# Kernel tuning notes

Hardware: AMD Instinct MI355X
Metric: run time of the kernel (lower is better)

Reference implementation:

```python
import jax, jax.numpy as jnp
import numpy as np

DIM = 512
HEADS = 16
HEAD_DIM = DIM // HEADS
SCALE = HEAD_DIM ** -0.5           # qk_scale defaults to head_dim**-0.5
W_GAIN = 1.0 / np.sqrt(DIM)        # FullyConnectedLayer weight_gain (lr_multiplier=1)


def _fc(x, w, b):
    # FullyConnectedLayer: x @ (w * weight_gain).T + b  (linear activation, bias_gain=1)
    return x @ (w * W_GAIN).T + b


def setup_inputs() -> dict:
    key = jax.random.key(0)
    ks = jax.random.split(key, 12)
    B_, N = 2048, 64
    nW = 64
    x = jax.random.normal(ks[0], (B_, N, DIM), dtype=jnp.float32)
    mask = jax.random.normal(ks[1], (nW, N, N), dtype=jnp.float32)
    mask_windows = jax.random.randint(ks[2], (B_, N, 1), 0, 2).astype(jnp.float32)
    # learned params: torch.randn init for weights, bias init 0
    qw = jax.random.normal(ks[3], (DIM, DIM), dtype=jnp.float32)
    kw = jax.random.normal(ks[4], (DIM, DIM), dtype=jnp.float32)
    vw = jax.random.normal(ks[5], (DIM, DIM), dtype=jnp.float32)
    pw = jax.random.normal(ks[6], (DIM, DIM), dtype=jnp.float32)
    qb = jnp.zeros((DIM,), jnp.float32)
    kb = jnp.zeros((DIM,), jnp.float32)
    vb = jnp.zeros((DIM,), jnp.float32)
    pb = jnp.zeros((DIM,), jnp.float32)
    return {"x": x, "mask": mask, "mask_windows": mask_windows,
            "qw": qw, "qb": qb, "kw": kw, "kb": kb,
            "vw": vw, "vb": vb, "pw": pw, "pb": pb}


def reference(x, mask, mask_windows, qw, qb, kw, kb, vw, vb, pw, pb):
    B, N, C = x.shape
    H, hd = HEADS, HEAD_DIM
    # F.normalize(p=2, dim=-1) with eps=1e-12 clamp on the norm
    norm = jnp.maximum(jnp.linalg.norm(x, axis=-1, keepdims=True), 1e-12)
    nx = x / norm
    q = _fc(nx, qw, qb).reshape(B, N, H, hd).transpose(0, 2, 1, 3)   # bhnd
    k = _fc(nx, kw, kb).reshape(B, N, H, hd).transpose(0, 2, 3, 1)   # bhdn
    v = _fc(x, vw, vb).reshape(B, N, H, hd).transpose(0, 2, 1, 3)    # bhnd
    attn = (q @ k) * SCALE                                           # [B,H,N,N]
    # shifted-window additive mask, broadcast over heads
    nW = mask.shape[0]
    attn = attn.reshape(B // nW, nW, H, N, N) + mask[None, :, None, :, :]
    attn = attn.reshape(B, H, N, N)
    # token-validity mask: 0 -> -100, 1 -> 0 (values are exactly 0/1)
    amw = mask_windows[:, :, 0][:, None, None, :]                    # [B,1,1,N]
    attn = attn + jnp.where(amw == 0, jnp.float32(-100.0), jnp.float32(0.0))
    attn = jax.nn.softmax(attn, axis=-1)
    out = (attn @ v).transpose(0, 2, 1, 3).reshape(B, N, C)
    out = _fc(out, pw, pb)
    # updated mask_windows (no-grad path in original)
    mw = jnp.clip(jnp.sum(mask_windows, axis=1, keepdims=True), 0.0, 1.0)  # [B,1,1]
    mw = jnp.tile(mw, (1, N, 1))                                           # [B,N,1]
    return out, mw
```

## Files before the change

kernel.cpp:

```cpp
#include <hip/hip_runtime.h>
#include <hip/hip_bf16.h>
#include <stdint.h>

typedef __bf16 bf16_t;
typedef bf16_t bf16x8 __attribute__((ext_vector_type(8)));
typedef float  f32x4  __attribute__((ext_vector_type(4)));

#define DEV static __device__ __forceinline__

constexpr int   BATCH  = 2048;
constexpr int   SEQ    = 64;
constexpr int   DIMC   = 512;
constexpr int   HEADS  = 16;
constexpr int   M_ROWS = BATCH * SEQ;
constexpr float W_GAIN = 0.044194173824159216f;
constexpr float QK_SCALE = 0.17677669529663687f;

DEV void async_copy16(const void* gp, void* lp) {
  __builtin_amdgcn_global_load_lds((__attribute__((address_space(1))) void*)(gp),
                                   (__attribute__((address_space(3))) void*)(lp),
                                   16, 0, 0);
}

DEV f32x4 mfma16(bf16x8 a, bf16x8 b, f32x4 c) {
  return __builtin_amdgcn_mfma_f32_16x16x32_bf16(a, b, c, 0, 0, 0);
}

__global__ __launch_bounds__(256) void k_prep(const float* __restrict__ x,
                                              bf16_t* __restrict__ nx,
                                              float* __restrict__ norms) {
  const int wid = threadIdx.x >> 6, lane = threadIdx.x & 63;
  const int row = blockIdx.x * 4 + wid;
  const float4* xr = (const float4*)(x + (size_t)row * DIMC);
  float4 v0 = xr[lane * 2 + 0];
  float4 v1 = xr[lane * 2 + 1];
  float ss = v0.x*v0.x + v0.y*v0.y + v0.z*v0.z + v0.w*v0.w
           + v1.x*v1.x + v1.y*v1.y + v1.z*v1.z + v1.w*v1.w;
#pragma unroll
  for (int o = 1; o < 64; o <<= 1) ss += __shfl_xor(ss, o);
  const float nrm = fmaxf(sqrtf(ss), 1e-12f);
  const float inv = 1.0f / nrm;
  bf16x8 o;
  o[0] = (bf16_t)(v0.x * inv); o[1] = (bf16_t)(v0.y * inv);
  o[2] = (bf16_t)(v0.z * inv); o[3] = (bf16_t)(v0.w * inv);
  o[4] = (bf16_t)(v1.x * inv); o[5] = (bf16_t)(v1.y * inv);
  o[6] = (bf16_t)(v1.z * inv); o[7] = (bf16_t)(v1.w * inv);
  *(bf16x8*)(nx + (size_t)row * DIMC + lane * 8) = o;
  if (lane == 0) norms[row] = nrm;
}

__global__ __launch_bounds__(256) void k_convw(const float* __restrict__ qw,
                                               const float* __restrict__ kw,
                                               const float* __restrict__ vw,
                                               const float* __restrict__ pw,
                                               bf16_t* __restrict__ wqkv,
                                               bf16_t* __restrict__ pwb) {
  const int i = blockIdx.x * 256 + threadIdx.x;
  constexpr int QKV_ELEMS = 1536 * 512;
  if (i < QKV_ELEMS) {
    const int n = i >> 9;
    float v = (n < 512) ? qw[i] : (n < 1024) ? kw[i - 512 * 512] : vw[i - 1024 * 512];
    wqkv[i] = (bf16_t)(v * W_GAIN);
  } else {
    const int j = i - QKV_ELEMS;
    pwb[j] = (bf16_t)(pw[j] * W_GAIN);
  }
}

template <int MODE>
__global__ __launch_bounds__(256) void k_gemm(const bf16_t* __restrict__ A,
                                              const bf16_t* __restrict__ Bw,
                                              const float* __restrict__ norms,
                                              const float* __restrict__ qb,
                                              const float* __restrict__ kb,
                                              const float* __restrict__ vb,
                                              bf16_t* __restrict__ Cb,
                                              float* __restrict__ Cf,
                                              const float* __restrict__ pb,
                                              int ntiles_n) {
  __shared__ bf16_t As[128 * 32];
  __shared__ bf16_t Bs[128 * 32];
  const int tid  = threadIdx.x;
  const int wid  = tid >> 6, lane = tid & 63;
  const int tn   = blockIdx.x % ntiles_n;
  const int tm   = blockIdx.x / ntiles_n;
  const int m0   = tm * 128, n0 = tn * 128;
  const int c    = lane & 15, g = lane >> 4;
  const int wr   = (wid >> 1) * 64, wc = (wid & 1) * 64;
  const int sr0  = wid * 16 + (lane >> 2);
  const int kc8  = (lane & 3) * 8;

  f32x4 acc[4][4] = {};

  for (int kt = 0; kt < 16; ++kt) {
    const int k0 = kt * 32;
    async_copy16(A  + (size_t)(m0 + sr0)      * 512 + k0 + kc8, &As[(wid    ) * 512]);
    async_copy16(A  + (size_t)(m0 + 64 + sr0) * 512 + k0 + kc8, &As[(4 + wid) * 512]);
    async_copy16(Bw + (size_t)(n0 + sr0)      * 512 + k0 + kc8, &Bs[(wid    ) * 512]);
    async_copy16(Bw + (size_t)(n0 + 64 + sr0) * 512 + k0 + kc8, &Bs[(4 + wid) * 512]);
    __syncthreads();

    bf16x8 af[4], bfr[4];
#pragma unroll
    for (int mi = 0; mi < 4; ++mi)
      af[mi] = *(const bf16x8*)&As[(wr + mi * 16 + c) * 32 + g * 8];
#pragma unroll
    for (int nj = 0; nj < 4; ++nj)
      bfr[nj] = *(const bf16x8*)&Bs[(wc + nj * 16 + c) * 32 + g * 8];
#pragma unroll
    for (int mi = 0; mi < 4; ++mi)
#pragma unroll
      for (int nj = 0; nj < 4; ++nj)
        acc[mi][nj] = mfma16(af[mi], bfr[nj], acc[mi][nj]);
    __syncthreads();
  }

  if (MODE == 0) {
#pragma unroll
    for (int mi = 0; mi < 4; ++mi) {
#pragma unroll
      for (int r = 0; r < 4; ++r) {
        const int gm = m0 + wr + mi * 16 + g * 4 + r;
        const float nrm = norms[gm];
#pragma unroll
        for (int nj = 0; nj < 4; ++nj) {
          const int gn = n0 + wc + nj * 16 + c;
          const float bias = (gn < 512) ? qb[gn] : (gn < 1024) ? kb[gn - 512] : vb[gn - 1024];
          float v = acc[mi][nj][r];
          if (gn >= 1024) v *= nrm;
          v += bias;
          Cb[(size_t)gm * 1536 + gn] = (bf16_t)v;
        }
      }
    }
  } else {
#pragma unroll
    for (int mi = 0; mi < 4; ++mi)
#pragma unroll
      for (int nj = 0; nj < 4; ++nj) {
        const int gn = n0 + wc + nj * 16 + c;
        const float bias = pb[gn];
#pragma unroll
        for (int r = 0; r < 4; ++r) {
          const int gm = m0 + wr + mi * 16 + g * 4 + r;
          Cf[(size_t)gm * 512 + gn] = acc[mi][nj][r] + bias;
        }
      }
  }
}

__global__ __launch_bounds__(256) void k_attn(const bf16_t* __restrict__ qkv,
                                              const float* __restrict__ wmask,
                                              const float* __restrict__ mwin,
                                              bf16_t* __restrict__ aout) {
  __shared__ bf16_t Pl[4][64 * 72];
  __shared__ bf16_t Vl[4][64 * 34];
  const int wid = threadIdx.x >> 6, lane = threadIdx.x & 63;
  const int gw  = blockIdx.x * 4 + wid;
  const int b   = gw >> 4, h = gw & 15;
  const int c   = lane & 15, g = lane >> 4;
  const size_t base = (size_t)b * 64 * 1536;

  bf16x8 qa[4], kf[4];
#pragma unroll
  for (int mi = 0; mi < 4; ++mi)
    qa[mi] = *(const bf16x8*)(qkv + base + (size_t)(mi * 16 + c) * 1536 + h * 32 + g * 8);
#pragma unroll
  for (int nj = 0; nj < 4; ++nj)
    kf[nj] = *(const bf16x8*)(qkv + base + (size_t)(nj * 16 + c) * 1536 + 512 + h * 32 + g * 8);

  {
    const int jr = lane >> 2;
    const int c8 = (lane & 3) * 8;
#pragma unroll
    for (int t = 0; t < 4; ++t) {
      const int row = jr + t * 16;
      bf16x8 v = *(const bf16x8*)(qkv + base + (size_t)row * 1536 + 1024 + h * 32 + c8);
      uint32_t* dst = (uint32_t*)&Vl[wid][row * 34 + c8];
      const uint32_t* src = (const uint32_t*)&v;
      dst[0] = src[0]; dst[1] = src[1]; dst[2] = src[2]; dst[3] = src[3];
    }
  }

  f32x4 s[4][4];
  const f32x4 zero = {0.f, 0.f, 0.f, 0.f};
#pragma unroll
  for (int mi = 0; mi < 4; ++mi)
#pragma unroll
    for (int nj = 0; nj < 4; ++nj)
      s[mi][nj] = mfma16(qa[mi], kf[nj], zero);

  float kadd[4];
#pragma unroll
  for (int nj = 0; nj < 4; ++nj) {
    const float mv = mwin[b * 64 + nj * 16 + c];
    kadd[nj] = (mv == 0.0f) ? -100.0f : 0.0f;
  }
  const int w = b & 63;
  const float* wm = wmask + (size_t)w * 4096;
#pragma unroll
  for (int mi = 0; mi < 4; ++mi)
#pragma unroll
    for (int nj = 0; nj < 4; ++nj)
#pragma unroll
      for (int r = 0; r < 4; ++r) {
        const int i = mi * 16 + g * 4 + r;
        s[mi][nj][r] = s[mi][nj][r] * QK_SCALE + wm[i * 64 + nj * 16 + c] + kadd[nj];
      }

#pragma unroll
  for (int mi = 0; mi < 4; ++mi)
#pragma unroll
    for (int r = 0; r < 4; ++r) {
      float mx = fmaxf(fmaxf(s[mi][0][r], s[mi][1][r]), fmaxf(s[mi][2][r], s[mi][3][r]));
#pragma unroll
      for (int o = 1; o < 16; o <<= 1) mx = fmaxf(mx, __shfl_xor(mx, o));
      float sum = 0.f;
#pragma unroll
      for (int nj = 0; nj < 4; ++nj) {
        const float p = __expf(s[mi][nj][r] - mx);
        s[mi][nj][r] = p;
        sum += p;
      }
#pragma unroll
      for (int o = 1; o < 16; o <<= 1) sum += __shfl_xor(sum, o);
      const float inv = 1.0f / sum;
#pragma unroll
      for (int nj = 0; nj < 4; ++nj) s[mi][nj][r] *= inv;
    }

#pragma unroll
  for (int mi = 0; mi < 4; ++mi)
#pragma unroll
    for (int nj = 0; nj < 4; ++nj)
#pragma unroll
      for (int r = 0; r < 4; ++r) {
        const int i = mi * 16 + g * 4 + r, j = nj * 16 + c;
        Pl[wid][i * 72 + j] = (bf16_t)s[mi][nj][r];
      }
  f32x4 o[4][2] = {};
#pragma unroll
  for (int ks = 0; ks < 2; ++ks) {
    bf16x8 pa[4];
#pragma unroll
    for (int mi = 0; mi < 4; ++mi)
      pa[mi] = *(const bf16x8*)&Pl[wid][(mi * 16 + c) * 72 + ks * 32 + g * 8];
#pragma unroll
    for (int nd = 0; nd < 2; ++nd) {
      bf16x8 vf;
#pragma unroll
      for (int t = 0; t < 8; ++t)
        vf[t] = Vl[wid][(ks * 32 + g * 8 + t) * 34 + nd * 16 + c];
#pragma unroll
      for (int mi = 0; mi < 4; ++mi)
        o[mi][nd] = mfma16(pa[mi], vf, o[mi][nd]);
    }
  }

  bf16_t* op = aout + (size_t)b * 64 * 512 + h * 32;
#pragma unroll
  for (int mi = 0; mi < 4; ++mi)
#pragma unroll
    for (int nd = 0; nd < 2; ++nd)
#pragma unroll
      for (int r = 0; r < 4; ++r) {
        const int i = mi * 16 + g * 4 + r;
        op[(size_t)i * 512 + nd * 16 + c] = (bf16_t)o[mi][nd][r];
      }
}

__global__ __launch_bounds__(256) void k_mw(const float* __restrict__ mwin,
                                            float* __restrict__ outmw) {
  const int wid = threadIdx.x >> 6, lane = threadIdx.x & 63;
  const int b = blockIdx.x * 4 + wid;
  float v = mwin[b * 64 + lane];
#pragma unroll
  for (int o = 1; o < 64; o <<= 1) v += __shfl_xor(v, o);
  outmw[b * 64 + lane] = fminf(fmaxf(v, 0.0f), 1.0f);
}

extern "C" void kernel_launch(void* const* d_in, const int* in_sizes, int n_in,
                              void* d_out, int out_size, void* d_ws, size_t ws_size,
                              hipStream_t stream) {
  const float* x    = (const float*)d_in[0];
  const float* mask = (const float*)d_in[1];
  const float* mwin = (const float*)d_in[2];
  const float* qw   = (const float*)d_in[3];
  const float* qb   = (const float*)d_in[4];
  const float* kw   = (const float*)d_in[5];
  const float* kb   = (const float*)d_in[6];
  const float* vw   = (const float*)d_in[7];
  const float* vb   = (const float*)d_in[8];
  const float* pw   = (const float*)d_in[9];
  const float* pb   = (const float*)d_in[10];

  float* out   = (float*)d_out;
  float* outmw = out + (size_t)M_ROWS * DIMC;

  char* ws = (char*)d_ws;
  float*  norms = (float*) (ws);
  bf16_t* wqkv  = (bf16_t*)(ws + 524288);
  bf16_t* pwb   = (bf16_t*)(ws + 2097152);
  bf16_t* nx    = (bf16_t*)(ws + 2621440);
  bf16_t* qkv   = (bf16_t*)(ws + 136839168);
  bf16_t* aout  = nx;

  k_convw<<<4096, 256, 0, stream>>>(qw, kw, vw, pw, wqkv, pwb);
  k_prep<<<M_ROWS / 4, 256, 0, stream>>>(x, nx, norms);
  k_gemm<0><<<(M_ROWS / 128) * 12, 256, 0, stream>>>(nx, wqkv, norms, qb, kb, vb,
                                                     qkv, nullptr, nullptr, 12);
  k_attn<<<BATCH * HEADS / 4, 256, 0, stream>>>(qkv, mask, mwin, aout);
  k_gemm<1><<<(M_ROWS / 128) * 4, 256, 0, stream>>>(aout, pwb, nullptr, nullptr, nullptr, nullptr,
                                                    nullptr, out, pb, 4);
  k_mw<<<BATCH / 4, 256, 0, stream>>>(mwin, outmw);
}
```

Measured before the change: 1.372 ms.

## Write V transposed from QKV GEMM, double-buffer GEMM tiles, swizzle block order

The QKV GEMM epilogue now writes V into a per-window, per-head transposed layout in a separate buffer. Q and K go to a narrower 1024-column buffer. The attention kernel can then load V fragments straight from global memory as vectors, with no LDS staging and no scalar gather. The GEMM main loop also double-buffers its LDS tiles so the next K-slice load is issued before computing the current one, and block indices are remapped in groups of eight to change tile scheduling order. Costs are twice the GEMM LDS footprint, a less coalesced 8-byte scattered store for V, and dependence on barrier semantics to complete the async copies.

```diff
diff --git a/kernel.cpp b/kernel.cpp
--- a/kernel.cpp
+++ b/kernel.cpp
@@ -4,6 +4,7 @@
 
 typedef __bf16 bf16_t;
 typedef bf16_t bf16x8 __attribute__((ext_vector_type(8)));
+typedef bf16_t bf16x4 __attribute__((ext_vector_type(4)));
 typedef float  f32x4  __attribute__((ext_vector_type(4)));
 
 #define DEV static __device__ __forceinline__
@@ -75,15 +76,18 @@
                                               const float* __restrict__ kb,
                                               const float* __restrict__ vb,
                                               bf16_t* __restrict__ Cb,
+                                              bf16_t* __restrict__ vT,
                                               float* __restrict__ Cf,
                                               const float* __restrict__ pb,
                                               int ntiles_n) {
-  __shared__ bf16_t As[128 * 32];
-  __shared__ bf16_t Bs[128 * 32];
+  __shared__ bf16_t As[2][128 * 32];
+  __shared__ bf16_t Bs[2][128 * 32];
   const int tid  = threadIdx.x;
   const int wid  = tid >> 6, lane = tid & 63;
-  const int tn   = blockIdx.x % ntiles_n;
-  const int tm   = blockIdx.x / ntiles_n;
+  int bid = blockIdx.x;
+  bid = (bid & 7) * ((int)gridDim.x >> 3) + (bid >> 3);
+  const int tn   = bid % ntiles_n;
+  const int tm   = bid / ntiles_n;
   const int m0   = tm * 128, n0 = tn * 128;
   const int c    = lane & 15, g = lane >> 4;
   const int wr   = (wid >> 1) * 64, wc = (wid & 1) * 64;
@@ -92,21 +96,28 @@
 
   f32x4 acc[4][4] = {};
 
+  auto stage = [&](int buf, int kt) {
+    const int k0 = kt * 32;
+    async_copy16(A  + (size_t)(m0 + sr0)      * 512 + k0 + kc8, &As[buf][(wid    ) * 512]);
+    async_copy16(A  + (size_t)(m0 + 64 + sr0) * 512 + k0 + kc8, &As[buf][(4 + wid) * 512]);
+    async_copy16(Bw + (size_t)(n0 + sr0)      * 512 + k0 + kc8, &Bs[buf][(wid    ) * 512]);
+    async_copy16(Bw + (size_t)(n0 + 64 + sr0) * 512 + k0 + kc8, &Bs[buf][(4 + wid) * 512]);
+  };
+
+  stage(0, 0);
+  __syncthreads();
+
+#pragma unroll 2
   for (int kt = 0; kt < 16; ++kt) {
-    const int k0 = kt * 32;
-    async_copy16(A  + (size_t)(m0 + sr0)      * 512 + k0 + kc8, &As[(wid    ) * 512]);
-    async_copy16(A  + (size_t)(m0 + 64 + sr0) * 512 + k0 + kc8, &As[(4 + wid) * 512]);
-    async_copy16(Bw + (size_t)(n0 + sr0)      * 512 + k0 + kc8, &Bs[(wid    ) * 512]);
-    async_copy16(Bw + (size_t)(n0 + 64 + sr0) * 512 + k0 + kc8, &Bs[(4 + wid) * 512]);
-    __syncthreads();
-
+    const int cur = kt & 1;
+    if (kt + 1 < 16) stage(cur ^ 1, kt + 1);
     bf16x8 af[4], bfr[4];
 #pragma unroll
     for (int mi = 0; mi < 4; ++mi)
-      af[mi] = *(const bf16x8*)&As[(wr + mi * 16 + c) * 32 + g * 8];
+      af[mi] = *(const bf16x8*)&As[cur][(wr + mi * 16 + c) * 32 + g * 8];
 #pragma unroll
     for (int nj = 0; nj < 4; ++nj)
-      bfr[nj] = *(const bf16x8*)&Bs[(wc + nj * 16 + c) * 32 + g * 8];
+      bfr[nj] = *(const bf16x8*)&Bs[cur][(wc + nj * 16 + c) * 32 + g * 8];
 #pragma unroll
     for (int mi = 0; mi < 4; ++mi)
 #pragma unroll
@@ -116,22 +127,37 @@
   }
 
   if (MODE == 0) {
-#pragma unroll
-    for (int mi = 0; mi < 4; ++mi) {
-#pragma unroll
-      for (int r = 0; r < 4; ++r) {
-        const int gm = m0 + wr + mi * 16 + g * 4 + r;
-        const float nrm = norms[gm];
+    if (n0 >= 1024) {
+      const int bwin = (m0 + wr) >> 6;
+#pragma unroll
+      for (int nj = 0; nj < 4; ++nj) {
+        const int gnv = (n0 - 1024) + wc + nj * 16 + c;
+        const int hh = gnv >> 5, dd = gnv & 31;
+        const float bias = vb[gnv];
+#pragma unroll
+        for (int mi = 0; mi < 4; ++mi) {
+          bf16x4 pack;
+#pragma unroll
+          for (int r = 0; r < 4; ++r) {
+            const int gm = m0 + wr + mi * 16 + g * 4 + r;
+            pack[r] = (bf16_t)(acc[mi][nj][r] * norms[gm] + bias);
+          }
+          *(bf16x4*)&vT[(((size_t)bwin * 16 + hh) * 32 + dd) * 64 + mi * 16 + g * 4] = pack;
+        }
+      }
+    } else {
+#pragma unroll
+      for (int mi = 0; mi < 4; ++mi)
 #pragma unroll
         for (int nj = 0; nj < 4; ++nj) {
           const int gn = n0 + wc + nj * 16 + c;
-          const float bias = (gn < 512) ? qb[gn] : (gn < 1024) ? kb[gn - 512] : vb[gn - 1024];
-          float v = acc[mi][nj][r];
-          if (gn >= 1024) v *= nrm;
-          v += bias;
-          Cb[(size_t)gm * 1536 + gn] = (bf16_t)v;
+          const float bias = (gn < 512) ? qb[gn] : kb[gn - 512];
+#pragma unroll
+          for (int r = 0; r < 4; ++r) {
+            const int gm = m0 + wr + mi * 16 + g * 4 + r;
+            Cb[(size_t)gm * 1024 + gn] = (bf16_t)(acc[mi][nj][r] + bias);
+          }
         }
-      }
     }
   } else {
 #pragma unroll
@@ -149,38 +175,25 @@
   }
 }
 
-__global__ __launch_bounds__(256) void k_attn(const bf16_t* __restrict__ qkv,
+__global__ __launch_bounds__(256) void k_attn(const bf16_t* __restrict__ qk,
+                                              const bf16_t* __restrict__ vT,
                                               const float* __restrict__ wmask,
                                               const float* __restrict__ mwin,
                                               bf16_t* __restrict__ aout) {
   __shared__ bf16_t Pl[4][64 * 72];
-  __shared__ bf16_t Vl[4][64 * 34];
   const int wid = threadIdx.x >> 6, lane = threadIdx.x & 63;
   const int gw  = blockIdx.x * 4 + wid;
   const int b   = gw >> 4, h = gw & 15;
   const int c   = lane & 15, g = lane >> 4;
-  const size_t base = (size_t)b * 64 * 1536;
+  const size_t base = (size_t)b * 64 * 1024;
 
   bf16x8 qa[4], kf[4];
 #pragma unroll
   for (int mi = 0; mi < 4; ++mi)
-    qa[mi] = *(const bf16x8*)(qkv + base + (size_t)(mi * 16 + c) * 1536 + h * 32 + g * 8);
+    qa[mi] = *(const bf16x8*)(qk + base + (size_t)(mi * 16 + c) * 1024 + h * 32 + g * 8);
 #pragma unroll
   for (int nj = 0; nj < 4; ++nj)
-    kf[nj] = *(const bf16x8*)(qkv + base + (size_t)(nj * 16 + c) * 1536 + 512 + h * 32 + g * 8);
-
-  {
-    const int jr = lane >> 2;
-    const int c8 = (lane & 3) * 8;
-#pragma unroll
-    for (int t = 0; t < 4; ++t) {
-      const int row = jr + t * 16;
-      bf16x8 v = *(const bf16x8*)(qkv + base + (size_t)row * 1536 + 1024 + h * 32 + c8);
-      uint32_t* dst = (uint32_t*)&Vl[wid][row * 34 + c8];
-      const uint32_t* src = (const uint32_t*)&v;
-      dst[0] = src[0]; dst[1] = src[1]; dst[2] = src[2]; dst[3] = src[3];
-    }
-  }
+    kf[nj] = *(const bf16x8*)(qk + base + (size_t)(nj * 16 + c) * 1024 + 512 + h * 32 + g * 8);
 
   f32x4 s[4][4];
   const f32x4 zero = {0.f, 0.f, 0.f, 0.f};
@@ -189,6 +202,14 @@
 #pragma unroll
     for (int nj = 0; nj < 4; ++nj)
       s[mi][nj] = mfma16(qa[mi], kf[nj], zero);
+
+  bf16x8 vf[2][2];
+#pragma unroll
+  for (int ks = 0; ks < 2; ++ks)
+#pragma unroll
+    for (int nd = 0; nd < 2; ++nd)
+      vf[ks][nd] = *(const bf16x8*)&vT[(((size_t)b * 16 + h) * 32 + nd * 16 + c) * 64
+                                       + ks * 32 + g * 8];
 
   float kadd[4];
 #pragma unroll
@@ -246,15 +267,10 @@
     for (int mi = 0; mi < 4; ++mi)
       pa[mi] = *(const bf16x8*)&Pl[wid][(mi * 16 + c) * 72 + ks * 32 + g * 8];
 #pragma unroll
-    for (int nd = 0; nd < 2; ++nd) {
-      bf16x8 vf;
-#pragma unroll
-      for (int t = 0; t < 8; ++t)
-        vf[t] = Vl[wid][(ks * 32 + g * 8 + t) * 34 + nd * 16 + c];
+    for (int nd = 0; nd < 2; ++nd)
 #pragma unroll
       for (int mi = 0; mi < 4; ++mi)
-        o[mi][nd] = mfma16(pa[mi], vf, o[mi][nd]);
-    }
+        o[mi][nd] = mfma16(pa[mi], vf[ks][nd], o[mi][nd]);
   }
 
   bf16_t* op = aout + (size_t)b * 64 * 512 + h * 32;
@@ -302,15 +318,16 @@
   bf16_t* wqkv  = (bf16_t*)(ws + 524288);
   bf16_t* pwb   = (bf16_t*)(ws + 2097152);
   bf16_t* nx    = (bf16_t*)(ws + 2621440);
-  bf16_t* qkv   = (bf16_t*)(ws + 136839168);
+  bf16_t* qk    = (bf16_t*)(ws + 136839168);
+  bf16_t* vT    = (bf16_t*)(ws + 405274624);
   bf16_t* aout  = nx;
 
   k_convw<<<4096, 256, 0, stream>>>(qw, kw, vw, pw, wqkv, pwb);
   k_prep<<<M_ROWS / 4, 256, 0, stream>>>(x, nx, norms);
   k_gemm<0><<<(M_ROWS / 128) * 12, 256, 0, stream>>>(nx, wqkv, norms, qb, kb, vb,
-                                                     qkv, nullptr, nullptr, 12);
-  k_attn<<<BATCH * HEADS / 4, 256, 0, stream>>>(qkv, mask, mwin, aout);
+                                                     qk, vT, nullptr, nullptr, 12);
+  k_attn<<<BATCH * HEADS / 4, 256, 0, stream>>>(qk, vT, mask, mwin, aout);
   k_gemm<1><<<(M_ROWS / 128) * 4, 256, 0, stream>>>(aout, pwb, nullptr, nullptr, nullptr, nullptr,
-                                                    nullptr, out, pb, 4);
+                                                    nullptr, nullptr, out, pb, 4);
   k_mw<<<BATCH / 4, 256, 0, stream>>>(mwin, outmw);
 }
```

Result: faster. 1.138 ms (-17.1%).
